# Performance work log

Measured on AMD Instinct MI355X. Metric: run time of the kernel, lower is better.

## Reference

```python
import jax, jax.numpy as jnp
import numpy as np

# Model dims (match init_kwargs)
N = 150            # n_constituents
P = 16             # len(params)
HID = 50           # hidden
DE = 14            # De
DO = 10            # Do
NT = 5             # n_targets
B = 256            # batch
NR = N * (N - 1)   # 22350 directed edges


def _linear_params(key, fan_in, fan_out):
    # torch.nn.Linear default init: U(-1/sqrt(fan_in), 1/sqrt(fan_in))
    k1, k2 = jax.random.split(key)
    lim = 1.0 / np.sqrt(fan_in)
    W = jax.random.uniform(k1, (fan_out, fan_in), minval=-lim, maxval=lim, dtype=jnp.float32)
    b = jax.random.uniform(k2, (fan_out,), minval=-lim, maxval=lim, dtype=jnp.float32)
    return W, b


def setup_inputs() -> dict:
    key = jax.random.key(0)
    ks = jax.random.split(key, 10)
    # Edge list: itertools.product(range(N), range(N)) with r != s; Rr one-hot on r, Rs on s.
    pairs = np.array([(r, s) for r in range(N) for s in range(N) if r != s], dtype=np.int32)
    recv = jnp.asarray(pairs[:, 0])  # [NR]
    send = jnp.asarray(pairs[:, 1])  # [NR]

    x = jax.random.normal(ks[0], (B, P, N), dtype=jnp.float32)

    fr1_w, fr1_b = _linear_params(ks[1], 2 * P, HID)
    fr2_w, fr2_b = _linear_params(ks[2], HID, HID // 2)
    fr3_w, fr3_b = _linear_params(ks[3], HID // 2, DE)
    fo1_w, fo1_b = _linear_params(ks[4], P + DE, HID)
    fo2_w, fo2_b = _linear_params(ks[5], HID, HID // 2)
    fo3_w, fo3_b = _linear_params(ks[6], HID // 2, DO)
    fc1_w, fc1_b = _linear_params(ks[7], DO * N, HID)
    fc2_w, fc2_b = _linear_params(ks[8], HID, HID // 2)
    fc3_w, fc3_b = _linear_params(ks[9], HID // 2, NT)

    return dict(x=x, recv=recv, send=send,
                fr1_w=fr1_w, fr1_b=fr1_b, fr2_w=fr2_w, fr2_b=fr2_b, fr3_w=fr3_w, fr3_b=fr3_b,
                fo1_w=fo1_w, fo1_b=fo1_b, fo2_w=fo2_w, fo2_b=fo2_b, fo3_w=fo3_w, fo3_b=fo3_b,
                fc1_w=fc1_w, fc1_b=fc1_b, fc2_w=fc2_w, fc2_b=fc2_b, fc3_w=fc3_w, fc3_b=fc3_b)


def reference(x, recv, send,
              fr1_w, fr1_b, fr2_w, fr2_b, fr3_w, fr3_b,
              fo1_w, fo1_b, fo2_w, fo2_b, fo3_w, fo3_b,
              fc1_w, fc1_b, fc2_w, fc2_b, fc3_w, fc3_b):
    relu = jax.nn.relu
    b = x.shape[0]
    # tmul(x, Rr/Rs) with one-hot Rr/Rs == gather along the node axis
    Orr = x[:, :, recv]                                   # (B, P, NR)
    Ors = x[:, :, send]                                   # (B, P, NR)
    Bm = jnp.concatenate([Orr, Ors], axis=1)              # (B, 2P, NR)
    Bm = jnp.transpose(Bm, (0, 2, 1))                     # (B, NR, 2P)
    # relational MLP fr (ReLU branch)
    h = relu(jnp.einsum('bef,hf->beh', Bm, fr1_w) + fr1_b)
    h = relu(jnp.einsum('beh,gh->beg', h, fr2_w) + fr2_b)
    E = relu(jnp.einsum('beg,dg->bed', h, fr3_w) + fr3_b)  # (B, NR, De)
    # tmul(E, Rr^T) == scatter-add edge effects onto receiver nodes
    Ebar = jnp.zeros((b, N, E.shape[-1]), x.dtype).at[:, recv].add(E)  # (B, N, De)
    C = jnp.concatenate([jnp.transpose(x, (0, 2, 1)), Ebar], axis=-1)  # (B, N, P+De)
    # object MLP fo
    h = relu(jnp.einsum('bnf,hf->bnh', C, fo1_w) + fo1_b)
    h = relu(jnp.einsum('bnh,gh->bng', h, fo2_w) + fo2_b)
    O = relu(jnp.einsum('bng,dg->bnd', h, fo3_w) + fo3_b)  # (B, N, Do)
    # classifier fc (sum_O=False: flatten N*Do)
    flat = O.reshape(b, N * O.shape[-1])
    h = relu(flat @ fc1_w.T + fc1_b)
    h = relu(h @ fc2_w.T + fc2_b)
    out = h @ fc3_w.T + fc3_b                              # (B, n_targets)
    return out
```

## Files before the change

kernel.cpp:

```cpp
#include <hip/hip_runtime.h>

#define N_   150
#define P_   16
#define DE_  14
#define DO_  10
#define NT_  5
#define B_   256
#define NRE  22350
#define H2_  25
#define HID_ 50

typedef float    f32x4 __attribute__((ext_vector_type(4)));
typedef _Float16 f16x8 __attribute__((ext_vector_type(8)));

typedef f16x8 f16x8_a __attribute__((may_alias));
typedef int2  int2_a  __attribute__((may_alias));
typedef f32x4 f32x4_a __attribute__((may_alias));

#define EBAR_OFF 0u
#define O_OFF    2457600u
#define XT_OFF   3225600u
#define W1E_OFF  4454400u
#define W1O_OFF  4458496u
#define W2E_OFF  4462592u
#define W2O_OFF  4466688u
#define W3E_OFF  4470784u
#define W3O_OFF  4471808u
#define B1E_OFF  4472832u
#define B1O_OFF  4473088u
#define B2E_OFF  4473344u
#define B2O_OFF  4473472u
#define B3E_OFF  4473600u
#define B3O_OFF  4473664u

__global__ __launch_bounds__(256) void prep_kernel(
    const float* __restrict__ x,
    const float* __restrict__ fr1_w, const float* __restrict__ fr1_b,
    const float* __restrict__ fr2_w, const float* __restrict__ fr2_b,
    const float* __restrict__ fr3_w, const float* __restrict__ fr3_b,
    const float* __restrict__ fo1_w, const float* __restrict__ fo1_b,
    const float* __restrict__ fo2_w, const float* __restrict__ fo2_b,
    const float* __restrict__ fo3_w, const float* __restrict__ fo3_b,
    char* __restrict__ ws)
{
    int tid = blockIdx.x * 256 + threadIdx.x;
    if (tid < 614400) {
        int b = tid / 2400; int rr = tid - b * 2400;
        int n = rr >> 4, p = rr & 15;
        ((_Float16*)(ws + XT_OFF))[tid] = (_Float16)x[b * 2400 + p * N_ + n];
        return;
    }
    int t = tid - 614400;
    if (t < 614400) { ((float*)(ws + EBAR_OFF))[t] = 0.f; return; }
    t -= 614400;
    if (t < 2048) { int n = t >> 5, k = t & 31;
        ((_Float16*)(ws + W1E_OFF))[t] = (_Float16)((n < 50) ? fr1_w[n * 32 + k] : 0.f); return; }
    t -= 2048;
    if (t < 2048) { int n = t >> 5, k = t & 31;
        ((_Float16*)(ws + W1O_OFF))[t] = (_Float16)((n < 50 && k < 30) ? fo1_w[n * 30 + k] : 0.f); return; }
    t -= 2048;
    if (t < 2048) { int n = t >> 6, k = t & 63;
        ((_Float16*)(ws + W2E_OFF))[t] = (_Float16)((n < 25 && k < 50) ? fr2_w[n * 50 + k] : 0.f); return; }
    t -= 2048;
    if (t < 2048) { int n = t >> 6, k = t & 63;
        ((_Float16*)(ws + W2O_OFF))[t] = (_Float16)((n < 25 && k < 50) ? fo2_w[n * 50 + k] : 0.f); return; }
    t -= 2048;
    if (t < 512) { int n = t >> 5, k = t & 31;
        ((_Float16*)(ws + W3E_OFF))[t] = (_Float16)((n < 14 && k < 25) ? fr3_w[n * 25 + k] : 0.f); return; }
    t -= 512;
    if (t < 512) { int n = t >> 5, k = t & 31;
        ((_Float16*)(ws + W3O_OFF))[t] = (_Float16)((n < 10 && k < 25) ? fo3_w[n * 25 + k] : 0.f); return; }
    t -= 512;
    if (t < 64) { ((float*)(ws + B1E_OFF))[t] = (t < 50) ? fr1_b[t] : 0.f; return; }
    t -= 64;
    if (t < 64) { ((float*)(ws + B1O_OFF))[t] = (t < 50) ? fo1_b[t] : 0.f; return; }
    t -= 64;
    if (t < 32) { ((float*)(ws + B2E_OFF))[t] = (t < 25) ? fr2_b[t] : 0.f; return; }
    t -= 32;
    if (t < 32) { ((float*)(ws + B2O_OFF))[t] = (t < 25) ? fo2_b[t] : 0.f; return; }
    t -= 32;
    if (t < 16) { ((float*)(ws + B3E_OFF))[t] = (t < 14) ? fr3_b[t] : 0.f; return; }
    t -= 16;
    if (t < 16) { ((float*)(ws + B3O_OFF))[t] = (t < 10) ? fo3_b[t] : 0.f; return; }
}

__device__ __forceinline__ unsigned pk2(float a, float b) {
    auto p = __builtin_amdgcn_cvt_pkrtz(a, b);
    return __builtin_bit_cast(unsigned, p);
}
__device__ __forceinline__ unsigned pkrelu(float a, float b) {
    return pk2(fmaxf(a, 0.f), fmaxf(b, 0.f));
}

__device__ __forceinline__ void flush_ebar(float* __restrict__ Ebar, int row,
                                           float acc, int lane) {
    acc += __shfl_xor(acc, 16);
    acc += __shfl_xor(acc, 32);
    if (lane < DE_) atomicAdd(&Ebar[row * 16 + lane], acc);
}

template<int TPW, bool OBJ>
__global__ __launch_bounds__(256) void mlp3_kernel(char* __restrict__ ws)
{
    const _Float16* __restrict__ xT = (const _Float16*)(ws + XT_OFF);
    const _Float16* __restrict__ W1 = (const _Float16*)(ws + (OBJ ? W1O_OFF : W1E_OFF));
    const _Float16* __restrict__ W2 = (const _Float16*)(ws + (OBJ ? W2O_OFF : W2E_OFF));
    const _Float16* __restrict__ W3 = (const _Float16*)(ws + (OBJ ? W3O_OFF : W3E_OFF));
    const float* __restrict__ b1 = (const float*)(ws + (OBJ ? B1O_OFF : B1E_OFF));
    const float* __restrict__ b2 = (const float*)(ws + (OBJ ? B2O_OFF : B2E_OFF));
    const float* __restrict__ b3 = (const float*)(ws + (OBJ ? B3O_OFF : B3E_OFF));
    float*     __restrict__ Ebar = (float*)(ws + EBAR_OFF);
    _Float16*  __restrict__ O    = (_Float16*)(ws + O_OFF);

    const int t = threadIdx.x;
    const int lane = t & 63, wid = t >> 6;
    const int e16 = lane & 15, g = lane >> 4;

    __shared__ __align__(16) char s_lds[4][3072];
    char* ldsw = s_lds[wid];
    const int wsub = (g >> 1) * 256 + e16 * 16 + (g & 1) * 8;
    char*       h1w = ldsw + wsub;
    char*       h2w = ldsw + 2048 + wsub;
    const int rsub = g * 256 + e16 * 16;
    const char* h1r = ldsw + rsub;
    const char* h2r = ldsw + 2048 + rsub;

    f16x8 A1[4], A2[2][2], A3;
#pragma unroll
    for (int nt = 0; nt < 4; ++nt)
        A1[nt] = *(const f16x8*)&W1[(nt * 16 + e16) * 32 + g * 8];
#pragma unroll
    for (int nt = 0; nt < 2; ++nt)
#pragma unroll
        for (int kt = 0; kt < 2; ++kt)
            A2[nt][kt] = *(const f16x8*)&W2[(nt * 16 + e16) * 64 + kt * 32 + g * 8];
    A3 = *(const f16x8*)&W3[e16 * 32 + g * 8];

    f32x4 C1[4], C2[2];
#pragma unroll
    for (int nt = 0; nt < 4; ++nt) C1[nt] = *(const f32x4*)&b1[nt * 16 + g * 4];
#pragma unroll
    for (int nt = 0; nt < 2; ++nt) C2[nt] = *(const f32x4*)&b2[nt * 16 + g * 4];
    const float b3v = b3[e16];
    const f32x4 C3 = { b3v, b3v, b3v, b3v };

    int b = 0, tile0;
    if constexpr (OBJ) {
        tile0 = blockIdx.x * 4 + wid;
    } else {
        b = blockIdx.x / 44;
        tile0 = (blockIdx.x % 44) * 32 + wid * TPW;
    }
    const _Float16* __restrict__ xTb = xT + b * 2400;

    int   cur_r = -1;
    float acc_r = 0.f;

    for (int tt = 0; tt < TPW; ++tt) {
        const int tile = tile0 + tt;
        if constexpr (!OBJ) { if (tile * 16 >= NRE) break; }

        f16x8 Bf;
        if constexpr (!OBJ) {
            int e = tile * 16 + e16;
            int ec = e < NRE ? e : NRE - 1;
            unsigned r = (unsigned)ec / 149u;
            unsigned sp = (unsigned)ec - r * 149u;
            int s = (int)sp + (sp >= r ? 1 : 0);
            int node = (g < 2) ? (int)r : s;
            Bf = *(const f16x8*)&xTb[node * 16 + (g & 1) * 8];
        } else {
            int m = tile * 16 + e16;
            if (g < 2) {
                Bf = *(const f16x8*)&xT[m * 16 + g * 8];
            } else {
                const float* ep = &Ebar[m * 16 + (g & 1) * 8];
                f32x4 u0 = *(const f32x4_a*)ep;
                f32x4 u1 = *(const f32x4_a*)(ep + 4);
                uint4 uw;
                uw.x = pk2(u0[0], u0[1]); uw.y = pk2(u0[2], u0[3]);
                uw.z = pk2(u1[0], u1[1]); uw.w = pk2(u1[2], u1[3]);
                Bf = __builtin_bit_cast(f16x8, uw);
            }
        }

#pragma unroll
        for (int nt = 0; nt < 4; ++nt) {
            f32x4 a = __builtin_amdgcn_mfma_f32_16x16x32_f16(A1[nt], Bf, C1[nt], 0, 0, 0);
            int2 pkw; pkw.x = (int)pkrelu(a[0], a[1]); pkw.y = (int)pkrelu(a[2], a[3]);
            *(int2_a*)(h1w + nt * 512) = pkw;
        }

        f16x8 Bf2a = *(const f16x8_a*)(h1r);
        f16x8 Bf2b = *(const f16x8_a*)(h1r + 1024);
#pragma unroll
        for (int nt = 0; nt < 2; ++nt) {
            f32x4 a = __builtin_amdgcn_mfma_f32_16x16x32_f16(A2[nt][0], Bf2a, C2[nt], 0, 0, 0);
            a = __builtin_amdgcn_mfma_f32_16x16x32_f16(A2[nt][1], Bf2b, a, 0, 0, 0);
            int2 pkw; pkw.x = (int)pkrelu(a[0], a[1]); pkw.y = (int)pkrelu(a[2], a[3]);
            *(int2_a*)(h2w + nt * 512) = pkw;
        }

        f16x8 Af3 = *(const f16x8_a*)(h2r);
        f32x4 acc3 = __builtin_amdgcn_mfma_f32_16x16x32_f16(Af3, A3, C3, 0, 0, 0);

        if constexpr (OBJ) {
            if (e16 < DO_) {
#pragma unroll
                for (int v = 0; v < 4; ++v)
                    O[(tile * 16 + g * 4 + v) * DO_ + e16] = (_Float16)fmaxf(acc3[v], 0.f);
            }
        } else {
            const int r0 = (tile * 16) / 149;
            const int rsplit = (r0 + 1) * 149;
            const bool two = (tile * 16 + 15) >= rsplit;

            if (r0 != cur_r) {
                if (cur_r >= 0) flush_ebar(Ebar, b * N_ + cur_r, acc_r, lane);
                acc_r = 0.f; cur_r = r0;
            }
            if (!two) {
                acc_r += fmaxf(acc3[0], 0.f) + fmaxf(acc3[1], 0.f)
                       + fmaxf(acc3[2], 0.f) + fmaxf(acc3[3], 0.f);
            } else {
                float sA = 0.f, sB = 0.f;
                const int ebase = tile * 16 + g * 4;
#pragma unroll
                for (int v = 0; v < 4; ++v) {
                    float val = fmaxf(acc3[v], 0.f);
                    if (ebase + v >= rsplit) sB += val; else sA += val;
                }
                acc_r += sA;
                flush_ebar(Ebar, b * N_ + r0, acc_r, lane);
                acc_r = sB; cur_r = r0 + 1;
            }
        }
    }
    if constexpr (!OBJ) {
        if (cur_r >= 0 && cur_r < N_) flush_ebar(Ebar, b * N_ + cur_r, acc_r, lane);
    }
}

__global__ __launch_bounds__(256) void classifier_kernel(
    const _Float16* __restrict__ O,
    const float* __restrict__ fc1_w, const float* __restrict__ fc1_b,
    const float* __restrict__ fc2_w, const float* __restrict__ fc2_b,
    const float* __restrict__ fc3_w, const float* __restrict__ fc3_b,
    float* __restrict__ out)
{
    __shared__ float s_o[N_ * DO_];
    __shared__ float s_part[4][HID_];
    __shared__ float s_h1[HID_];
    __shared__ float s_h2[H2_];

    const int b = blockIdx.x;
    const int t = threadIdx.x;
    const int lane = t & 63, w = t >> 6;

    const _Float16* Ob = O + b * (N_ * DO_);
    for (int k = t; k < N_ * DO_; k += 256) s_o[k] = (float)Ob[k];
    __syncthreads();

    float acc[HID_];
#pragma unroll
    for (int i = 0; i < HID_; ++i) acc[i] = 0.0f;

    for (int kb = 0; kb < N_ * DO_; kb += 256) {
        int k = kb + t;
        if (k < N_ * DO_) {
            float o = s_o[k];
#pragma unroll
            for (int i = 0; i < HID_; ++i)
                acc[i] = fmaf(fc1_w[i * (N_ * DO_) + k], o, acc[i]);
        }
    }

#pragma unroll
    for (int i = 0; i < HID_; ++i) {
        float v = acc[i];
#pragma unroll
        for (int off = 32; off >= 1; off >>= 1) v += __shfl_xor(v, off);
        if (lane == i) s_part[w][i] = v;
    }
    __syncthreads();

    if (t < HID_) {
        float v = s_part[0][t] + s_part[1][t] + s_part[2][t] + s_part[3][t] + fc1_b[t];
        s_h1[t] = fmaxf(v, 0.0f);
    }
    __syncthreads();
    if (t < H2_) {
        float a = fc2_b[t];
#pragma unroll
        for (int k = 0; k < HID_; ++k) a = fmaf(fc2_w[t * HID_ + k], s_h1[k], a);
        s_h2[t] = fmaxf(a, 0.0f);
    }
    __syncthreads();
    if (t < NT_) {
        float a = fc3_b[t];
#pragma unroll
        for (int k = 0; k < H2_; ++k) a = fmaf(fc3_w[t * H2_ + k], s_h2[k], a);
        out[b * NT_ + t] = a;
    }
}

extern "C" void kernel_launch(void* const* d_in, const int* in_sizes, int n_in,
                              void* d_out, int out_size, void* d_ws, size_t ws_size,
                              hipStream_t stream) {
    const float* x     = (const float*)d_in[0];
    const float* fr1_w = (const float*)d_in[3];
    const float* fr1_b = (const float*)d_in[4];
    const float* fr2_w = (const float*)d_in[5];
    const float* fr2_b = (const float*)d_in[6];
    const float* fr3_w = (const float*)d_in[7];
    const float* fr3_b = (const float*)d_in[8];
    const float* fo1_w = (const float*)d_in[9];
    const float* fo1_b = (const float*)d_in[10];
    const float* fo2_w = (const float*)d_in[11];
    const float* fo2_b = (const float*)d_in[12];
    const float* fo3_w = (const float*)d_in[13];
    const float* fo3_b = (const float*)d_in[14];
    const float* fc1_w = (const float*)d_in[15];
    const float* fc1_b = (const float*)d_in[16];
    const float* fc2_w = (const float*)d_in[17];
    const float* fc2_b = (const float*)d_in[18];
    const float* fc3_w = (const float*)d_in[19];
    const float* fc3_b = (const float*)d_in[20];

    char* ws = (char*)d_ws;
    float* out = (float*)d_out;

    prep_kernel<<<4837, 256, 0, stream>>>(x, fr1_w, fr1_b, fr2_w, fr2_b, fr3_w, fr3_b,
                                          fo1_w, fo1_b, fo2_w, fo2_b, fo3_w, fo3_b, ws);
    mlp3_kernel<8, false><<<B_ * 44, 256, 0, stream>>>(ws);
    mlp3_kernel<1, true ><<<600, 256, 0, stream>>>(ws);
    classifier_kernel<<<B_, 256, 0, stream>>>((const _Float16*)(ws + O_OFF),
                                              fc1_w, fc1_b, fc2_w, fc2_b, fc3_w, fc3_b, out);
}
```

Before: 139.0 us.

## Restructure edge MLP per receiver with hoisted receiver-half layer-1 product

The edge kernel now gives each wave a fixed set of receiver nodes and loops over all 160 padded sender slots. The receiver half of layer 1 is computed once per receiver as a 16x16x16 MFMA bias and reused across the sender tiles. Results are summed in registers with DPP reductions and written directly into Ebar, so the atomics and the Ebar zeroing in prep go away. This removes the per-edge index division, redundant receiver-side FLOPs and atomic contention. In exchange it does padded work on 10 extra slots (the self edge and the tail) that must be masked, and it relies on a fixed grid-to-receiver mapping.

After: 111.8 us. 1.24x faster.

```diff
diff --git a/kernel.cpp b/kernel.cpp
--- a/kernel.cpp
+++ b/kernel.cpp
@@ -9,11 +9,14 @@
 #define NRE  22350
 #define H2_  25
 #define HID_ 50
+#define RPW  5
 
 typedef float    f32x4 __attribute__((ext_vector_type(4)));
 typedef _Float16 f16x8 __attribute__((ext_vector_type(8)));
+typedef _Float16 f16x4 __attribute__((ext_vector_type(4)));
 
 typedef f16x8 f16x8_a __attribute__((may_alias));
+typedef f16x4 f16x4_a __attribute__((may_alias));
 typedef int2  int2_a  __attribute__((may_alias));
 typedef f32x4 f32x4_a __attribute__((may_alias));
 
@@ -51,8 +54,6 @@
         return;
     }
     int t = tid - 614400;
-    if (t < 614400) { ((float*)(ws + EBAR_OFF))[t] = 0.f; return; }
-    t -= 614400;
     if (t < 2048) { int n = t >> 5, k = t & 31;
         ((_Float16*)(ws + W1E_OFF))[t] = (_Float16)((n < 50) ? fr1_w[n * 32 + k] : 0.f); return; }
     t -= 2048;
@@ -88,32 +89,147 @@
     auto p = __builtin_amdgcn_cvt_pkrtz(a, b);
     return __builtin_bit_cast(unsigned, p);
 }
-__device__ __forceinline__ unsigned pkrelu(float a, float b) {
-    return pk2(fmaxf(a, 0.f), fmaxf(b, 0.f));
-}
-
-__device__ __forceinline__ void flush_ebar(float* __restrict__ Ebar, int row,
-                                           float acc, int lane) {
-    acc += __shfl_xor(acc, 16);
-    acc += __shfl_xor(acc, 32);
-    if (lane < DE_) atomicAdd(&Ebar[row * 16 + lane], acc);
-}
-
-template<int TPW, bool OBJ>
-__global__ __launch_bounds__(256) void mlp3_kernel(char* __restrict__ ws)
+__device__ __forceinline__ unsigned pkmax0(unsigned x, unsigned z) {
+    unsigned r;
+    asm("v_pk_max_f16 %0, %1, %2" : "=v"(r) : "v"(x), "v"(z));
+    return r;
+}
+
+template<int CTRL>
+__device__ __forceinline__ float dppadd(float v) {
+    int s = __builtin_amdgcn_update_dpp(0, __builtin_bit_cast(int, v), CTRL, 0xF, 0xF, true);
+    return v + __builtin_bit_cast(float, s);
+}
+__device__ __forceinline__ float dpp_sum16(float v) {
+    v = dppadd<0x121>(v);
+    v = dppadd<0x122>(v);
+    v = dppadd<0x124>(v);
+    v = dppadd<0x128>(v);
+    return v;
+}
+
+__global__ __launch_bounds__(256) void edge_kernel(char* __restrict__ ws)
 {
     const _Float16* __restrict__ xT = (const _Float16*)(ws + XT_OFF);
-    const _Float16* __restrict__ W1 = (const _Float16*)(ws + (OBJ ? W1O_OFF : W1E_OFF));
-    const _Float16* __restrict__ W2 = (const _Float16*)(ws + (OBJ ? W2O_OFF : W2E_OFF));
-    const _Float16* __restrict__ W3 = (const _Float16*)(ws + (OBJ ? W3O_OFF : W3E_OFF));
-    const float* __restrict__ b1 = (const float*)(ws + (OBJ ? B1O_OFF : B1E_OFF));
-    const float* __restrict__ b2 = (const float*)(ws + (OBJ ? B2O_OFF : B2E_OFF));
-    const float* __restrict__ b3 = (const float*)(ws + (OBJ ? B3O_OFF : B3E_OFF));
-    float*     __restrict__ Ebar = (float*)(ws + EBAR_OFF);
-    _Float16*  __restrict__ O    = (_Float16*)(ws + O_OFF);
-
-    const int t = threadIdx.x;
-    const int lane = t & 63, wid = t >> 6;
+    const _Float16* __restrict__ W1 = (const _Float16*)(ws + W1E_OFF);
+    const _Float16* __restrict__ W2 = (const _Float16*)(ws + W2E_OFF);
+    const _Float16* __restrict__ W3 = (const _Float16*)(ws + W3E_OFF);
+    const float* __restrict__ b1 = (const float*)(ws + B1E_OFF);
+    const float* __restrict__ b2 = (const float*)(ws + B2E_OFF);
+    const float* __restrict__ b3 = (const float*)(ws + B3E_OFF);
+    float* __restrict__ Ebar = (float*)(ws + EBAR_OFF);
+
+    const int t = threadIdx.x, lane = t & 63, wid = t >> 6;
+    const int e16 = lane & 15, g = lane >> 4;
+
+    __shared__ __align__(16) char s_lds[4][6144];
+    char* L = s_lds[wid];
+
+    const int gw = blockIdx.x * 4 + wid;
+    const int b  = gw / 30;
+    const int r0 = (gw - b * 30) * RPW;
+
+    f16x4 A1r[4], A1s[4];
+#pragma unroll
+    for (int nt = 0; nt < 4; ++nt) {
+        A1r[nt] = *(const f16x4*)&W1[(nt * 16 + e16) * 32 + g * 4];
+        A1s[nt] = *(const f16x4*)&W1[(nt * 16 + e16) * 32 + 16 + g * 4];
+    }
+    f16x8 A2f[2][2], A3f;
+#pragma unroll
+    for (int nt = 0; nt < 2; ++nt)
+#pragma unroll
+        for (int kt = 0; kt < 2; ++kt)
+            A2f[nt][kt] = *(const f16x8*)&W2[(nt * 16 + e16) * 64 + kt * 32 + g * 8];
+    A3f = *(const f16x8*)&W3[e16 * 32 + g * 8];
+
+    f32x4 Cb1[4], Cb2[2], Cb3;
+#pragma unroll
+    for (int nt = 0; nt < 4; ++nt) Cb1[nt] = *(const f32x4*)&b1[nt * 16 + g * 4];
+#pragma unroll
+    for (int nt = 0; nt < 2; ++nt) Cb2[nt] = *(const f32x4*)&b2[nt * 16 + g * 4];
+    Cb3 = *(const f32x4*)&b3[g * 4];
+
+    const char* xTb = (const char*)xT + b * 4800;
+    const int laneoff = e16 * 32 + g * 8;
+    const int wsub = (g >> 1) * 256 + e16 * 16 + 8 * (g & 1);
+    const int rsub = g * 256 + e16 * 16;
+    const unsigned zu = 0;
+
+    for (int rr = 0; rr < RPW; ++rr) {
+        const int r = r0 + rr;
+
+        f16x4 Bxr = *(const f16x4_a*)(xTb + r * 32 + g * 8);
+        f32x4 H1P[4];
+#pragma unroll
+        for (int nt = 0; nt < 4; ++nt)
+            H1P[nt] = __builtin_amdgcn_mfma_f32_16x16x16f16(A1r[nt], Bxr, Cb1[nt], 0, 0, 0);
+
+        const int ktile = r >> 4, klane = r & 15;
+        float ac0 = 0.f, ac1 = 0.f, ac2 = 0.f, ac3 = 0.f;
+
+#pragma unroll 2
+        for (int tile = 0; tile < 10; ++tile) {
+            char* h1b = L + (tile & 1) * 3072;
+            char* h2b = h1b + 2048;
+
+            f16x4 Bxs = *(const f16x4_a*)(xTb + tile * 512 + laneoff);
+
+#pragma unroll
+            for (int nt = 0; nt < 4; ++nt) {
+                f32x4 d1 = __builtin_amdgcn_mfma_f32_16x16x16f16(A1s[nt], Bxs, H1P[nt], 0, 0, 0);
+                int2 pw;
+                pw.x = (int)pkmax0(pk2(d1[0], d1[1]), zu);
+                pw.y = (int)pkmax0(pk2(d1[2], d1[3]), zu);
+                *(int2_a*)(h1b + nt * 512 + wsub) = pw;
+            }
+
+            f16x8 B2a = *(const f16x8_a*)(h1b + rsub);
+            f16x8 B2b = *(const f16x8_a*)(h1b + 1024 + rsub);
+#pragma unroll
+            for (int nt = 0; nt < 2; ++nt) {
+                f32x4 d2 = __builtin_amdgcn_mfma_f32_16x16x32_f16(A2f[nt][0], B2a, Cb2[nt], 0, 0, 0);
+                d2 = __builtin_amdgcn_mfma_f32_16x16x32_f16(A2f[nt][1], B2b, d2, 0, 0, 0);
+                int2 pw;
+                pw.x = (int)pkmax0(pk2(d2[0], d2[1]), zu);
+                pw.y = (int)pkmax0(pk2(d2[2], d2[3]), zu);
+                *(int2_a*)(h2b + nt * 512 + wsub) = pw;
+            }
+
+            f16x8 B3f = *(const f16x8_a*)(h2b + rsub);
+            f32x4 d3 = __builtin_amdgcn_mfma_f32_16x16x32_f16(A3f, B3f, Cb3, 0, 0, 0);
+
+            float v0 = fmaxf(d3[0], 0.f), v1 = fmaxf(d3[1], 0.f);
+            float v2 = fmaxf(d3[2], 0.f), v3 = fmaxf(d3[3], 0.f);
+            if (tile == ktile || tile == 9) {
+                bool kill = (tile == ktile && e16 == klane) || (tile == 9 && e16 >= 6);
+                if (kill) { v0 = 0.f; v1 = 0.f; v2 = 0.f; v3 = 0.f; }
+            }
+            ac0 += v0; ac1 += v1; ac2 += v2; ac3 += v3;
+        }
+
+        ac0 = dpp_sum16(ac0); ac1 = dpp_sum16(ac1);
+        ac2 = dpp_sum16(ac2); ac3 = dpp_sum16(ac3);
+        if (e16 == 0) {
+            f32x4 o = { ac0, ac1, ac2, ac3 };
+            *(f32x4_a*)&Ebar[(b * 150 + r) * 16 + g * 4] = o;
+        }
+    }
+}
+
+__global__ __launch_bounds__(256) void obj_kernel(char* __restrict__ ws)
+{
+    const _Float16* __restrict__ xT = (const _Float16*)(ws + XT_OFF);
+    const _Float16* __restrict__ W1 = (const _Float16*)(ws + W1O_OFF);
+    const _Float16* __restrict__ W2 = (const _Float16*)(ws + W2O_OFF);
+    const _Float16* __restrict__ W3 = (const _Float16*)(ws + W3O_OFF);
+    const float* __restrict__ b1 = (const float*)(ws + B1O_OFF);
+    const float* __restrict__ b2 = (const float*)(ws + B2O_OFF);
+    const float* __restrict__ b3 = (const float*)(ws + B3O_OFF);
+    const float* __restrict__ Ebar = (const float*)(ws + EBAR_OFF);
+    _Float16* __restrict__ O = (_Float16*)(ws + O_OFF);
+
+    const int t = threadIdx.x, lane = t & 63, wid = t >> 6;
     const int e16 = lane & 15, g = lane >> 4;
 
     __shared__ __align__(16) char s_lds[4][3072];
@@ -143,101 +259,50 @@
     for (int nt = 0; nt < 2; ++nt) C2[nt] = *(const f32x4*)&b2[nt * 16 + g * 4];
     const float b3v = b3[e16];
     const f32x4 C3 = { b3v, b3v, b3v, b3v };
-
-    int b = 0, tile0;
-    if constexpr (OBJ) {
-        tile0 = blockIdx.x * 4 + wid;
+    const unsigned zu = 0;
+
+    const int tile = blockIdx.x * 4 + wid;
+    const int m = tile * 16 + e16;
+
+    f16x8 Bf;
+    if (g < 2) {
+        Bf = *(const f16x8*)&xT[m * 16 + g * 8];
     } else {
-        b = blockIdx.x / 44;
-        tile0 = (blockIdx.x % 44) * 32 + wid * TPW;
-    }
-    const _Float16* __restrict__ xTb = xT + b * 2400;
-
-    int   cur_r = -1;
-    float acc_r = 0.f;
-
-    for (int tt = 0; tt < TPW; ++tt) {
-        const int tile = tile0 + tt;
-        if constexpr (!OBJ) { if (tile * 16 >= NRE) break; }
-
-        f16x8 Bf;
-        if constexpr (!OBJ) {
-            int e = tile * 16 + e16;
-            int ec = e < NRE ? e : NRE - 1;
-            unsigned r = (unsigned)ec / 149u;
-            unsigned sp = (unsigned)ec - r * 149u;
-            int s = (int)sp + (sp >= r ? 1 : 0);
-            int node = (g < 2) ? (int)r : s;
-            Bf = *(const f16x8*)&xTb[node * 16 + (g & 1) * 8];
-        } else {
-            int m = tile * 16 + e16;
-            if (g < 2) {
-                Bf = *(const f16x8*)&xT[m * 16 + g * 8];
-            } else {
-                const float* ep = &Ebar[m * 16 + (g & 1) * 8];
-                f32x4 u0 = *(const f32x4_a*)ep;
-                f32x4 u1 = *(const f32x4_a*)(ep + 4);
-                uint4 uw;
-                uw.x = pk2(u0[0], u0[1]); uw.y = pk2(u0[2], u0[3]);
-                uw.z = pk2(u1[0], u1[1]); uw.w = pk2(u1[2], u1[3]);
-                Bf = __builtin_bit_cast(f16x8, uw);
-            }
-        }
-
-#pragma unroll
-        for (int nt = 0; nt < 4; ++nt) {
-            f32x4 a = __builtin_amdgcn_mfma_f32_16x16x32_f16(A1[nt], Bf, C1[nt], 0, 0, 0);
-            int2 pkw; pkw.x = (int)pkrelu(a[0], a[1]); pkw.y = (int)pkrelu(a[2], a[3]);
-            *(int2_a*)(h1w + nt * 512) = pkw;
-        }
-
-        f16x8 Bf2a = *(const f16x8_a*)(h1r);
-        f16x8 Bf2b = *(const f16x8_a*)(h1r + 1024);
-#pragma unroll
-        for (int nt = 0; nt < 2; ++nt) {
-            f32x4 a = __builtin_amdgcn_mfma_f32_16x16x32_f16(A2[nt][0], Bf2a, C2[nt], 0, 0, 0);
-            a = __builtin_amdgcn_mfma_f32_16x16x32_f16(A2[nt][1], Bf2b, a, 0, 0, 0);
-            int2 pkw; pkw.x = (int)pkrelu(a[0], a[1]); pkw.y = (int)pkrelu(a[2], a[3]);
-            *(int2_a*)(h2w + nt * 512) = pkw;
-        }
-
-        f16x8 Af3 = *(const f16x8_a*)(h2r);
-        f32x4 acc3 = __builtin_amdgcn_mfma_f32_16x16x32_f16(Af3, A3, C3, 0, 0, 0);
-
-        if constexpr (OBJ) {
-            if (e16 < DO_) {
-#pragma unroll
-                for (int v = 0; v < 4; ++v)
-                    O[(tile * 16 + g * 4 + v) * DO_ + e16] = (_Float16)fmaxf(acc3[v], 0.f);
-            }
-        } else {
-            const int r0 = (tile * 16) / 149;
-            const int rsplit = (r0 + 1) * 149;
-            const bool two = (tile * 16 + 15) >= rsplit;
-
-            if (r0 != cur_r) {
-                if (cur_r >= 0) flush_ebar(Ebar, b * N_ + cur_r, acc_r, lane);
-                acc_r = 0.f; cur_r = r0;
-            }
-            if (!two) {
-                acc_r += fmaxf(acc3[0], 0.f) + fmaxf(acc3[1], 0.f)
-                       + fmaxf(acc3[2], 0.f) + fmaxf(acc3[3], 0.f);
-            } else {
-                float sA = 0.f, sB = 0.f;
-                const int ebase = tile * 16 + g * 4;
-#pragma unroll
-                for (int v = 0; v < 4; ++v) {
-                    float val = fmaxf(acc3[v], 0.f);
-                    if (ebase + v >= rsplit) sB += val; else sA += val;
-                }
-                acc_r += sA;
-                flush_ebar(Ebar, b * N_ + r0, acc_r, lane);
-                acc_r = sB; cur_r = r0 + 1;
-            }
-        }
-    }
-    if constexpr (!OBJ) {
-        if (cur_r >= 0 && cur_r < N_) flush_ebar(Ebar, b * N_ + cur_r, acc_r, lane);
+        const float* ep = &Ebar[m * 16 + (g & 1) * 8];
+        f32x4 u0 = *(const f32x4_a*)ep;
+        f32x4 u1 = *(const f32x4_a*)(ep + 4);
+        uint4 uw;
+        uw.x = pk2(u0[0], u0[1]); uw.y = pk2(u0[2], u0[3]);
+        uw.z = pk2(u1[0], u1[1]); uw.w = pk2(u1[2], u1[3]);
+        Bf = __builtin_bit_cast(f16x8, uw);
+    }
+
+#pragma unroll
+    for (int nt = 0; nt < 4; ++nt) {
+        f32x4 a = __builtin_amdgcn_mfma_f32_16x16x32_f16(A1[nt], Bf, C1[nt], 0, 0, 0);
+        int2 pw;
+        pw.x = (int)pkmax0(pk2(a[0], a[1]), zu);
+        pw.y = (int)pkmax0(pk2(a[2], a[3]), zu);
+        *(int2_a*)(h1w + nt * 512) = pw;
+    }
+    f16x8 B2a = *(const f16x8_a*)(h1r);
+    f16x8 B2b = *(const f16x8_a*)(h1r + 1024);
+#pragma unroll
+    for (int nt = 0; nt < 2; ++nt) {
+        f32x4 a = __builtin_amdgcn_mfma_f32_16x16x32_f16(A2[nt][0], B2a, C2[nt], 0, 0, 0);
+        a = __builtin_amdgcn_mfma_f32_16x16x32_f16(A2[nt][1], B2b, a, 0, 0, 0);
+        int2 pw;
+        pw.x = (int)pkmax0(pk2(a[0], a[1]), zu);
+        pw.y = (int)pkmax0(pk2(a[2], a[3]), zu);
+        *(int2_a*)(h2w + nt * 512) = pw;
+    }
+    f16x8 Af3 = *(const f16x8_a*)(h2r);
+    f32x4 acc3 = __builtin_amdgcn_mfma_f32_16x16x32_f16(Af3, A3, C3, 0, 0, 0);
+
+    if (e16 < DO_) {
+#pragma unroll
+        for (int v = 0; v < 4; ++v)
+            O[(tile * 16 + g * 4 + v) * DO_ + e16] = (_Float16)fmaxf(acc3[v], 0.f);
     }
 }
 
@@ -330,10 +395,10 @@
     char* ws = (char*)d_ws;
     float* out = (float*)d_out;
 
-    prep_kernel<<<4837, 256, 0, stream>>>(x, fr1_w, fr1_b, fr2_w, fr2_b, fr3_w, fr3_b,
+    prep_kernel<<<2437, 256, 0, stream>>>(x, fr1_w, fr1_b, fr2_w, fr2_b, fr3_w, fr3_b,
                                           fo1_w, fo1_b, fo2_w, fo2_b, fo3_w, fo3_b, ws);
-    mlp3_kernel<8, false><<<B_ * 44, 256, 0, stream>>>(ws);
-    mlp3_kernel<1, true ><<<600, 256, 0, stream>>>(ws);
+    edge_kernel<<<1920, 256, 0, stream>>>(ws);
+    obj_kernel<<<600, 256, 0, stream>>>(ws);
     classifier_kernel<<<B_, 256, 0, stream>>>((const _Float16*)(ws + O_OFF),
                                               fc1_w, fc1_b, fc2_w, fc2_b, fc3_w, fc3_b, out);
 }
```
